# Performance work log

Measured on AMD Instinct MI355X. Metric: run time of the kernel, lower is better.

The kernel has to match this reference:

```python
import jax, jax.numpy as jnp
import numpy as np

IGNORE_INDEX = -100
FIXED_TAG_WEIGHT = 2.0
ALLOWED_TOKEN_WEIGHT = 1.5


def setup_inputs() -> dict:
    key = jax.random.key(0)
    k1, k2 = jax.random.split(key)
    B, S, V = 2, 2048, 32000
    logits = jax.random.normal(k1, (B, S, V), dtype=jnp.float32)
    # small id range so tag subsequence matches actually occur
    labels = jax.random.randint(k2, (B, S), 0, 20).astype(jnp.int64)
    tag0 = jnp.array([5, 6, 7], dtype=jnp.int64)       # e.g. tokenizer.encode('<think>')
    tag1 = jnp.array([10, 11], dtype=jnp.int64)        # e.g. tokenizer.encode('</think>')
    allowed_ids = jnp.array([3, 4], dtype=jnp.int64)   # single allowed color token ids
    return {"logits": logits, "labels": labels, "tag0": tag0, "tag1": tag1,
            "allowed_ids": allowed_ids}


def _covered(labels, tag):
    """Boolean [B,S] mask of positions covered by any occurrence of `tag` in labels."""
    B, S = labels.shape
    L = tag.shape[0]          # static (concrete tag length)
    n = S - L + 1             # number of sliding windows
    match = jnp.ones((B, n), dtype=bool)
    for k in range(L):        # L is tiny (2-3); unrolled, fully vectorized over B,S
        match = match & (labels[:, k:k + n] == tag[k])
    cov = jnp.zeros((B, S), dtype=bool)
    for k in range(L):        # dilate match to cover the full tag span
        cov = cov | jnp.pad(match, ((0, 0), (k, L - 1 - k)))
    return cov


def reference(logits, labels, tag0, tag1, allowed_ids):
    B, S = labels.shape
    weights = jnp.ones((B, S), dtype=jnp.float32)
    # fixed tags first (fixed_tag_weight > 1.0)
    for tag in (tag0, tag1):
        weights = jnp.where(_covered(labels, tag), FIXED_TAG_WEIGHT, weights)
    # allowed single-token ids (allowed_token_weight > 1.0), applied after, may overwrite
    allowed_hit = jnp.any(labels[..., None] == allowed_ids, axis=-1)
    weights = jnp.where(allowed_hit, ALLOWED_TOKEN_WEIGHT, weights)

    # ForCausalLMLoss: shift, CE with ignore_index=-100, mean over valid tokens
    shift_logits = logits[:, :-1, :]            # [B, S-1, V]
    shift_labels = labels[:, 1:]                # [B, S-1]
    logp = jax.nn.log_softmax(shift_logits, axis=-1)
    nll = -jnp.take_along_axis(logp, jnp.clip(shift_labels, 0)[..., None], axis=-1)[..., 0]
    valid = (shift_labels != IGNORE_INDEX).astype(nll.dtype)
    ce = jnp.sum(nll * valid) / jnp.maximum(jnp.sum(valid), 1.0)
    # torch code: (scalar_loss * weights.view(-1)).mean() == scalar_loss * weights.mean()
    return ce * jnp.mean(weights)
```

## Files before the change

### kernel.cpp

```cpp
#include <hip/hip_runtime.h>
#include <math.h>

static constexpr int kB = 2;
static constexpr int kS = 2048;
static constexpr int kV = 32000;
static constexpr int kIgnore = -100;
static constexpr float kTagW = 2.0f;
static constexpr float kAllowW = 1.5f;
static constexpr int kRows = kB * (kS - 1);

typedef float vf4 __attribute__((ext_vector_type(4)));


__global__ __launch_bounds__(256) void row_nll_kernel(
    const float* __restrict__ logits, const int* __restrict__ labels,
    float* __restrict__ ws) {
  const int row = blockIdx.x;
  const int b = row / (kS - 1);
  const int s = row - b * (kS - 1);
  const float* __restrict__ rowp = logits + (size_t)(b * kS + s) * kV;
  const vf4* __restrict__ row4 = (const vf4*)rowp;
  const int tid = threadIdx.x;

  float acc[8] = {0.f, 0.f, 0.f, 0.f, 0.f, 0.f, 0.f, 0.f};

  for (int o = 0; o < 3; ++o) {
    const int base = tid + o * 2048;
    vf4 v[8];
#pragma unroll
    for (int u = 0; u < 8; ++u)
      v[u] = row4[base + u * 256];
#pragma unroll
    for (int u = 0; u < 8; ++u)
      acc[u] += __expf(v[u].x) + __expf(v[u].y) + __expf(v[u].z) + __expf(v[u].w);
  }
  {
    const int base = tid + 6144;
    vf4 v[8];
#pragma unroll
    for (int u = 0; u < 8; ++u) {
      const int idx = base + u * 256;
      v[u] = row4[idx < 8000 ? idx : 0];
    }
#pragma unroll
    for (int u = 0; u < 8; ++u) {
      const int idx = base + u * 256;
      const float e =
          __expf(v[u].x) + __expf(v[u].y) + __expf(v[u].z) + __expf(v[u].w);
      acc[u] += (idx < 8000) ? e : 0.0f;
    }
  }

  float l = ((acc[0] + acc[1]) + (acc[2] + acc[3])) +
            ((acc[4] + acc[5]) + (acc[6] + acc[7]));

  for (int off = 32; off > 0; off >>= 1) l += __shfl_down(l, off, 64);

  __shared__ float sl[4];
  if ((tid & 63) == 0) sl[tid >> 6] = l;
  __syncthreads();

  if (tid == 0) {
    l = (sl[0] + sl[1]) + (sl[2] + sl[3]);
    const int lbl = labels[b * kS + s + 1];
    const int c = lbl < 0 ? 0 : lbl;
    ws[row] = __logf(l) - rowp[c];
  }
}

__device__ __forceinline__ bool covered_by(const int* __restrict__ lab, int s,
                                           const int* __restrict__ tag, int L) {
  bool cov = false;
  for (int k = 0; k < L; ++k) {
    const int st = s - k;
    if (st < 0 || st + L > kS) continue;
    bool match = true;
    for (int j = 0; j < L; ++j) match &= (lab[st + j] == tag[j]);
    cov |= match;
  }
  return cov;
}

__global__ __launch_bounds__(256) void weights_finalize_kernel(
    const int* __restrict__ labels,
    const int* __restrict__ tag0, int L0,
    const int* __restrict__ tag1, int L1,
    const int* __restrict__ allowed, int nA,
    const float* __restrict__ ws, float* __restrict__ out) {
  __shared__ int t0[16], t1[16], al[16];
  if (threadIdx.x < L0) t0[threadIdx.x] = tag0[threadIdx.x];
  if (threadIdx.x < L1) t1[threadIdx.x] = tag1[threadIdx.x];
  if (threadIdx.x < nA) al[threadIdx.x] = allowed[threadIdx.x];
  __syncthreads();

  float wsum = 0.0f;
  for (int idx = threadIdx.x; idx < kB * kS; idx += 256) {
    const int b = idx / kS;
    const int s = idx - b * kS;
    const int* __restrict__ lab = labels + b * kS;
    float w = 1.0f;
    if (covered_by(lab, s, t0, L0)) w = kTagW;
    if (covered_by(lab, s, t1, L1)) w = kTagW;
    const int me = lab[s];
    for (int a = 0; a < nA; ++a)
      if (me == al[a]) w = kAllowW;
    wsum += w;
  }

  float nsum = 0.0f, vcnt = 0.0f;
  for (int r = threadIdx.x; r < kRows; r += 256) {
    const int b = r / (kS - 1);
    const int s = r - b * (kS - 1);
    if (labels[b * kS + s + 1] != kIgnore) {
      nsum += ws[r];
      vcnt += 1.0f;
    }
  }

  for (int off = 32; off > 0; off >>= 1) {
    wsum += __shfl_down(wsum, off, 64);
    nsum += __shfl_down(nsum, off, 64);
    vcnt += __shfl_down(vcnt, off, 64);
  }
  __shared__ float pw[4], pn[4], pv[4];
  if ((threadIdx.x & 63) == 0) {
    pw[threadIdx.x >> 6] = wsum;
    pn[threadIdx.x >> 6] = nsum;
    pv[threadIdx.x >> 6] = vcnt;
  }
  __syncthreads();
  if (threadIdx.x == 0) {
    const float W = (pw[0] + pw[1]) + (pw[2] + pw[3]);
    const float N = (pn[0] + pn[1]) + (pn[2] + pn[3]);
    const float V = (pv[0] + pv[1]) + (pv[2] + pv[3]);
    out[0] = (N / fmaxf(V, 1.0f)) * (W * (1.0f / (float)(kB * kS)));
  }
}

extern "C" void kernel_launch(void* const* d_in, const int* in_sizes, int n_in,
                              void* d_out, int out_size, void* d_ws, size_t ws_size,
                              hipStream_t stream) {
  const float* logits = (const float*)d_in[0];
  const int* labels  = (const int*)d_in[1];
  const int* tag0    = (const int*)d_in[2];
  const int* tag1    = (const int*)d_in[3];
  const int* allowed = (const int*)d_in[4];
  float* ws  = (float*)d_ws;
  float* out = (float*)d_out;

  row_nll_kernel<<<kRows, 256, 0, stream>>>(logits, labels, ws);
  weights_finalize_kernel<<<1, 256, 0, stream>>>(labels, tag0, in_sizes[2],
                                                 tag1, in_sizes[3],
                                                 allowed, in_sizes[4], ws, out);
}
```

Measured before the change: 695.4 us.

## Use persistent grid-stride blocks with software-pipelined nontemporal row loads

Launches a fixed grid of 2048 persistent blocks, each looping over two rows instead of one block per row. Within a row, the next chunk's vector loads are issued before the exponentials of the current chunk are computed, to overlap memory latency with math. All loads use nontemporal hints so the streamed logits bypass cache retention. Costs more registers for the double buffer and adds an extra barrier per row iteration.

```diff
diff --git a/kernel.cpp b/kernel.cpp
--- a/kernel.cpp
+++ b/kernel.cpp
@@ -8,63 +8,75 @@
 static constexpr float kTagW = 2.0f;
 static constexpr float kAllowW = 1.5f;
 static constexpr int kRows = kB * (kS - 1);
+static constexpr int kGrid = 2048;
 
 typedef float vf4 __attribute__((ext_vector_type(4)));
 
 
+__device__ __forceinline__ float esum(vf4 v) {
+  return (__expf(v.x) + __expf(v.y)) + (__expf(v.z) + __expf(v.w));
+}
+
 __global__ __launch_bounds__(256) void row_nll_kernel(
     const float* __restrict__ logits, const int* __restrict__ labels,
     float* __restrict__ ws) {
-  const int row = blockIdx.x;
-  const int b = row / (kS - 1);
-  const int s = row - b * (kS - 1);
-  const float* __restrict__ rowp = logits + (size_t)(b * kS + s) * kV;
-  const vf4* __restrict__ row4 = (const vf4*)rowp;
   const int tid = threadIdx.x;
+  __shared__ float sl[4];
 
-  float acc[8] = {0.f, 0.f, 0.f, 0.f, 0.f, 0.f, 0.f, 0.f};
+  for (int row = blockIdx.x; row < kRows; row += kGrid) {
+    const int b = row / (kS - 1);
+    const int s = row - b * (kS - 1);
+    const float* __restrict__ rowp = logits + (size_t)(b * kS + s) * kV;
+    const vf4* __restrict__ row4 = (const vf4*)rowp;
 
-  for (int o = 0; o < 3; ++o) {
-    const int base = tid + o * 2048;
-    vf4 v[8];
+    float acc[8] = {0.f, 0.f, 0.f, 0.f, 0.f, 0.f, 0.f, 0.f};
+    vf4 v[8], w[8];
+
 #pragma unroll
     for (int u = 0; u < 8; ++u)
-      v[u] = row4[base + u * 256];
+      v[u] = __builtin_nontemporal_load(row4 + tid + u * 256);
+
 #pragma unroll
     for (int u = 0; u < 8; ++u)
-      acc[u] += __expf(v[u].x) + __expf(v[u].y) + __expf(v[u].z) + __expf(v[u].w);
-  }
-  {
-    const int base = tid + 6144;
-    vf4 v[8];
+      w[u] = __builtin_nontemporal_load(row4 + tid + 2048 + u * 256);
+#pragma unroll
+    for (int u = 0; u < 8; ++u) acc[u] += esum(v[u]);
+
+#pragma unroll
+    for (int u = 0; u < 8; ++u)
+      v[u] = __builtin_nontemporal_load(row4 + tid + 4096 + u * 256);
+#pragma unroll
+    for (int u = 0; u < 8; ++u) acc[u] += esum(w[u]);
+
 #pragma unroll
     for (int u = 0; u < 8; ++u) {
-      const int idx = base + u * 256;
-      v[u] = row4[idx < 8000 ? idx : 0];
+      const int idx = tid + 6144 + u * 256;
+      w[u] = __builtin_nontemporal_load(row4 + (idx < 8000 ? idx : 0));
     }
 #pragma unroll
+    for (int u = 0; u < 8; ++u) acc[u] += esum(v[u]);
+
+#pragma unroll
     for (int u = 0; u < 8; ++u) {
-      const int idx = base + u * 256;
-      const float e =
-          __expf(v[u].x) + __expf(v[u].y) + __expf(v[u].z) + __expf(v[u].w);
-      acc[u] += (idx < 8000) ? e : 0.0f;
+      const int idx = tid + 6144 + u * 256;
+      acc[u] += (idx < 8000) ? esum(w[u]) : 0.0f;
     }
-  }
 
-  float l = ((acc[0] + acc[1]) + (acc[2] + acc[3])) +
-            ((acc[4] + acc[5]) + (acc[6] + acc[7]));
+    float l = ((acc[0] + acc[1]) + (acc[2] + acc[3])) +
+              ((acc[4] + acc[5]) + (acc[6] + acc[7]));
 
-  for (int off = 32; off > 0; off >>= 1) l += __shfl_down(l, off, 64);
+    for (int off = 32; off > 0; off >>= 1) l += __shfl_down(l, off, 64);
 
-  __shared__ float sl[4];
-  if ((tid & 63) == 0) sl[tid >> 6] = l;
-  __syncthreads();
+    if ((tid & 63) == 0) sl[tid >> 6] = l;
+    __syncthreads();
 
-  if (tid == 0) {
-    l = (sl[0] + sl[1]) + (sl[2] + sl[3]);
-    const int lbl = labels[b * kS + s + 1];
-    const int c = lbl < 0 ? 0 : lbl;
-    ws[row] = __logf(l) - rowp[c];
+    if (tid == 0) {
+      l = (sl[0] + sl[1]) + (sl[2] + sl[3]);
+      const int lbl = labels[b * kS + s + 1];
+      const int c = lbl < 0 ? 0 : lbl;
+      ws[row] = __logf(l) - rowp[c];
+    }
+    __syncthreads();
   }
 }
 
@@ -148,7 +160,7 @@
   float* ws  = (float*)d_ws;
   float* out = (float*)d_out;
 
-  row_nll_kernel<<<kRows, 256, 0, stream>>>(logits, labels, ws);
+  row_nll_kernel<<<kGrid, 256, 0, stream>>>(logits, labels, ws);
   weights_finalize_kernel<<<1, 256, 0, stream>>>(labels, tag0, in_sizes[2],
                                                  tag1, in_sizes[3],
                                                  allowed, in_sizes[4], ws, out);
```

New measurement: 661.7 us. 4.8% less time.

## Split rows into segments with persistent grid and atomic exp-sum accumulation

Applied to the files above, without the earlier changes.

Each logits row is split into four segments processed by a fixed 2048-block grid-stride loop, with partial exp-sums combined by atomicAdd into a zero-initialised workspace. Loads use nontemporal hints, and the log and target-logit gather move into the single-block finalize kernel. The aim is better load balance and more memory-level parallelism than one block per row. In exchange it adds an init kernel launch, atomics, and a serial finalize that now does about 4K logs and scattered gathers in one block.

```diff
diff --git a/kernel.cpp b/kernel.cpp
--- a/kernel.cpp
+++ b/kernel.cpp
@@ -8,63 +8,54 @@
 static constexpr float kTagW = 2.0f;
 static constexpr float kAllowW = 1.5f;
 static constexpr int kRows = kB * (kS - 1);
+static constexpr int kSegF4 = 2000;
+static constexpr int kSegPerRow = 4;
+static constexpr int kNSeg = kRows * kSegPerRow;
+static constexpr int kGrid = 2048;
 
 typedef float vf4 __attribute__((ext_vector_type(4)));
 
 
-__global__ __launch_bounds__(256) void row_nll_kernel(
-    const float* __restrict__ logits, const int* __restrict__ labels,
-    float* __restrict__ ws) {
-  const int row = blockIdx.x;
-  const int b = row / (kS - 1);
-  const int s = row - b * (kS - 1);
-  const float* __restrict__ rowp = logits + (size_t)(b * kS + s) * kV;
-  const vf4* __restrict__ row4 = (const vf4*)rowp;
+
+__global__ __launch_bounds__(256) void ws_init_kernel(float* __restrict__ ws) {
+  const int i = blockIdx.x * 256 + threadIdx.x;
+  if (i < kRows) ws[i] = 0.0f;
+}
+
+__global__ __launch_bounds__(256) void row_expsum_kernel(
+    const float* __restrict__ logits, float* __restrict__ ws) {
   const int tid = threadIdx.x;
+  __shared__ float sl[4];
 
-  float acc[8] = {0.f, 0.f, 0.f, 0.f, 0.f, 0.f, 0.f, 0.f};
+  for (int seg = blockIdx.x; seg < kNSeg; seg += kGrid) {
+    const int row = seg >> 2;
+    const int soff = (seg & 3) * kSegF4;
+    const int b = row / (kS - 1);
+    const int s = row - b * (kS - 1);
+    const vf4* __restrict__ p =
+        (const vf4*)(logits + (size_t)(b * kS + s) * kV) + soff;
 
-  for (int o = 0; o < 3; ++o) {
-    const int base = tid + o * 2048;
-    vf4 v[8];
-#pragma unroll
-    for (int u = 0; u < 8; ++u)
-      v[u] = row4[base + u * 256];
-#pragma unroll
-    for (int u = 0; u < 8; ++u)
-      acc[u] += __expf(v[u].x) + __expf(v[u].y) + __expf(v[u].z) + __expf(v[u].w);
-  }
-  {
-    const int base = tid + 6144;
     vf4 v[8];
 #pragma unroll
     for (int u = 0; u < 8; ++u) {
-      const int idx = base + u * 256;
-      v[u] = row4[idx < 8000 ? idx : 0];
+      const int idx = tid + u * 256;
+      v[u] = __builtin_nontemporal_load(p + (idx < kSegF4 ? idx : 0));
     }
+    float acc = 0.0f;
 #pragma unroll
     for (int u = 0; u < 8; ++u) {
-      const int idx = base + u * 256;
-      const float e =
-          __expf(v[u].x) + __expf(v[u].y) + __expf(v[u].z) + __expf(v[u].w);
-      acc[u] += (idx < 8000) ? e : 0.0f;
+      const int idx = tid + u * 256;
+      const float e = (__expf(v[u].x) + __expf(v[u].y)) +
+                      (__expf(v[u].z) + __expf(v[u].w));
+      acc += (idx < kSegF4) ? e : 0.0f;
     }
-  }
 
-  float l = ((acc[0] + acc[1]) + (acc[2] + acc[3])) +
-            ((acc[4] + acc[5]) + (acc[6] + acc[7]));
-
-  for (int off = 32; off > 0; off >>= 1) l += __shfl_down(l, off, 64);
-
-  __shared__ float sl[4];
-  if ((tid & 63) == 0) sl[tid >> 6] = l;
-  __syncthreads();
-
-  if (tid == 0) {
-    l = (sl[0] + sl[1]) + (sl[2] + sl[3]);
-    const int lbl = labels[b * kS + s + 1];
-    const int c = lbl < 0 ? 0 : lbl;
-    ws[row] = __logf(l) - rowp[c];
+    for (int off = 32; off > 0; off >>= 1) acc += __shfl_down(acc, off, 64);
+    if ((tid & 63) == 0) sl[tid >> 6] = acc;
+    __syncthreads();
+    if (tid == 0)
+      atomicAdd(&ws[row], (sl[0] + sl[1]) + (sl[2] + sl[3]));
+    __syncthreads();
   }
 }
 
@@ -82,7 +73,7 @@
 }
 
 __global__ __launch_bounds__(256) void weights_finalize_kernel(
-    const int* __restrict__ labels,
+    const float* __restrict__ logits, const int* __restrict__ labels,
     const int* __restrict__ tag0, int L0,
     const int* __restrict__ tag1, int L1,
     const int* __restrict__ allowed, int nA,
@@ -111,8 +102,10 @@
   for (int r = threadIdx.x; r < kRows; r += 256) {
     const int b = r / (kS - 1);
     const int s = r - b * (kS - 1);
-    if (labels[b * kS + s + 1] != kIgnore) {
-      nsum += ws[r];
+    const int lbl = labels[b * kS + s + 1];
+    if (lbl != kIgnore) {
+      const int c = lbl < 0 ? 0 : lbl;
+      nsum += __logf(ws[r]) - logits[(size_t)(b * kS + s) * kV + c];
       vcnt += 1.0f;
     }
   }
@@ -148,8 +141,10 @@
   float* ws  = (float*)d_ws;
   float* out = (float*)d_out;
 
-  row_nll_kernel<<<kRows, 256, 0, stream>>>(logits, labels, ws);
-  weights_finalize_kernel<<<1, 256, 0, stream>>>(labels, tag0, in_sizes[2],
+  ws_init_kernel<<<(kRows + 255) / 256, 256, 0, stream>>>(ws);
+  row_expsum_kernel<<<kGrid, 256, 0, stream>>>(logits, ws);
+  weights_finalize_kernel<<<1, 256, 0, stream>>>(logits, labels,
+                                                 tag0, in_sizes[2],
                                                  tag1, in_sizes[3],
                                                  allowed, in_sizes[4], ws, out);
 }
```

Measured after the change: 685.0 us. Within noise of the previous version (-1.5%).
